# Performance work log

Hardware: AMD Instinct MI355X
Metric: run time of the kernel (lower is better)

The kernel has to match this reference:

```python
import jax, jax.numpy as jnp
import numpy as np

B, S, DIM = 2, 2048, 2048
NH, HD, HDR = 16, 128, 64
DCKV, DCQ = 512, 1536


def _lin(x, W, b):
    return x @ W.T + b


def _rotate_half(x):
    x1, x2 = jnp.split(x, 2, axis=-1)
    return jnp.concatenate([-x2, x1], axis=-1)


def _rope(x, cos, sin):
    # x: [..., s, hdr]; cos/sin: [s, hdr]
    return x * cos + _rotate_half(x) * sin


def setup_inputs() -> dict:
    key = jax.random.key(0)
    ks = jax.random.split(key, 20)
    sc = 0.02

    def w(k, shape):
        return (jax.random.normal(k, shape, jnp.float32) * sc)

    inp = {}
    inp['x'] = jax.random.normal(ks[0], (B, S, DIM), jnp.float32)
    # standard RoPE tables for the decoupled rotary dim
    inv_freq = 1.0 / (10000.0 ** (jnp.arange(0, HDR, 2, dtype=jnp.float32) / HDR))
    t = jnp.arange(S, dtype=jnp.float32)
    freqs = jnp.outer(t, inv_freq)                      # [S, HDR/2]
    emb = jnp.concatenate([freqs, freqs], axis=-1)      # [S, HDR]
    inp['freq_cos'] = jnp.cos(emb)
    inp['freq_sin'] = jnp.sin(emb)
    inp['W_dq'] = w(ks[1], (DCQ, DIM));  inp['b_dq'] = jnp.zeros((DCQ,), jnp.float32)
    inp['W_uq'] = w(ks[2], (NH * HD, DCQ)); inp['b_uq'] = jnp.zeros((NH * HD,), jnp.float32)
    inp['W_qr'] = w(ks[3], (NH * HDR, DCQ)); inp['b_qr'] = jnp.zeros((NH * HDR,), jnp.float32)
    inp['W_dkv'] = w(ks[4], (DCKV, DIM)); inp['b_dkv'] = jnp.zeros((DCKV,), jnp.float32)
    inp['W_uk'] = w(ks[5], (NH * HD, DCKV)); inp['b_uk'] = jnp.zeros((NH * HD,), jnp.float32)
    inp['W_uv'] = w(ks[6], (NH * HD, DCKV)); inp['b_uv'] = jnp.zeros((NH * HD,), jnp.float32)
    inp['W_kr'] = w(ks[7], (HDR, DIM)); inp['b_kr'] = jnp.zeros((HDR,), jnp.float32)
    inp['W_out'] = w(ks[8], (DIM, DIM)); inp['b_out'] = jnp.zeros((DIM,), jnp.float32)
    return inp


def reference(x, freq_cos, freq_sin,
              W_dq, b_dq, W_uq, b_uq, W_qr, b_qr,
              W_dkv, b_dkv, W_uk, b_uk, W_uv, b_uv,
              W_kr, b_kr, W_out, b_out):
    b, s, d = x.shape
    c_q = _lin(x, W_dq, b_dq)                                  # [b,s,dcq]
    c_kv = _lin(x, W_dkv, b_dkv)                               # [b,s,dckv]
    c_q_r = _lin(c_q, W_qr, b_qr).reshape(b, s, NH, HDR).transpose(0, 2, 1, 3)  # [b,nh,s,hdr]
    k_r = _lin(x, W_kr, b_kr)[:, None]                         # [b,1,s,hdr]
    cos = freq_cos[:s]
    sin = freq_sin[:s]
    r_q = _rope(c_q_r, cos, sin)
    r_k = _rope(k_r, cos, sin)
    r_q = r_q.transpose(0, 2, 1, 3).reshape(b, s, NH * HDR)    # [b,s,nh*hdr]
    r_k = r_k[:, 0]                                            # [b,s,hdr]
    q = jnp.concatenate([_lin(c_q, W_uq, b_uq), r_q], axis=-1)  # [b,s,nh*hd+nh*hdr]
    k_base = _lin(c_kv, W_uk, b_uk)                            # [b,s,nh*hd]
    v = _lin(c_kv, W_uv, b_uv)                                 # [b,s,nh*hd]
    r_k_exp = jnp.broadcast_to(r_k[:, :, None, :], (b, s, NH, HDR)).reshape(b, s, NH * HDR)
    k = jnp.concatenate([k_base, r_k_exp], axis=-1)
    # faithful to original: view the concat into nh chunks of (hd+hdr)
    q = q.reshape(b, s, NH, HD + HDR).transpose(0, 2, 1, 3)    # [b,nh,s,hd+hdr]
    k = k.reshape(b, s, NH, HD + HDR).transpose(0, 2, 1, 3)
    v = v.reshape(b, s, NH, HD).transpose(0, 2, 1, 3)          # [b,nh,s,hd]
    scale = 1.0 / np.float32(np.sqrt(HD + HDR))
    att = jnp.einsum('bhqd,bhkd->bhqk', q, k) * scale          # [b,nh,s,s]
    mask = jnp.tril(jnp.ones((s, s), dtype=bool))
    att = jnp.where(mask, att, jnp.float32(-jnp.inf))
    att = jax.nn.softmax(att, axis=-1)
    y = jnp.einsum('bhqk,bhkd->bhqd', att, v)                  # [b,nh,s,hd]
    y = y.transpose(0, 2, 1, 3).reshape(b, s, d)
    return _lin(y, W_out, b_out)
```

## Files before the change

kernel.cpp:

```cpp
#include <hip/hip_runtime.h>
#include <hip/hip_bf16.h>
#include <stdint.h>


typedef __bf16 bf16x8 __attribute__((ext_vector_type(8)));
typedef float  f32x4  __attribute__((ext_vector_type(4)));

__device__ __forceinline__ uint16_t f2bf(float f) {
    uint32_t u = __builtin_bit_cast(uint32_t, f);
    u = (u + 0x7FFFu + ((u >> 16) & 1u)) >> 16;
    return (uint16_t)u;
}
__device__ __forceinline__ float bf2f(uint16_t h) {
    uint32_t u = ((uint32_t)h) << 16;
    return __builtin_bit_cast(float, u);
}

typedef __attribute__((address_space(3))) uint32_t lds_u32_t;
typedef const __attribute__((address_space(1))) uint32_t glb_u32_t;

__device__ __forceinline__ void gld16(const void* g, const void* l) {
    __builtin_amdgcn_global_load_lds((glb_u32_t*)(uintptr_t)g,
                                     (lds_u32_t*)(uint32_t)(uintptr_t)l, 16, 0, 0);
}

__global__ __launch_bounds__(256)
void conv_kernel(const float* __restrict__ src, uint16_t* __restrict__ dst,
                 int n_src, int n_dst)
{
    int i = (blockIdx.x * 256 + threadIdx.x) << 2;
    if (i >= n_dst) return;
    ushort4 o;
    if (i < n_src) {
        float4 v = *(const float4*)(src + i);
        o.x = f2bf(v.x); o.y = f2bf(v.y); o.z = f2bf(v.z); o.w = f2bf(v.w);
    } else {
        o.x = 0; o.y = 0; o.z = 0; o.w = 0;
    }
    *(ushort4*)(dst + i) = o;
}

template<int MODE>
__global__ __launch_bounds__(256, 2)
void gemm_fused(const uint16_t* __restrict__ A, const uint16_t* __restrict__ W,
                const float* __restrict__ b0, const float* __restrict__ b1,
                const float* __restrict__ b2,
                const float* __restrict__ fc, const float* __restrict__ fs,
                void* __restrict__ O0, void* __restrict__ O1,
                int M, int N, int K, int lda, int s1, int s2)
{
    __shared__ __align__(16) uint16_t Alds[128 * 32];
    __shared__ __align__(16) uint16_t Blds[128 * 32];

    const int tid  = threadIdx.x;
    const int lane = tid & 63;
    const int wave = tid >> 6;
    const int wm   = wave >> 1;
    const int wn   = wave & 1;
    const int m0   = blockIdx.y << 7;
    const int n0   = blockIdx.x << 7;

    f32x4 acc[4][4];
    #pragma unroll
    for (int i = 0; i < 4; ++i)
        #pragma unroll
        for (int j = 0; j < 4; ++j)
            acc[i][j] = (f32x4){0.f, 0.f, 0.f, 0.f};

    const int r0 = (wave << 5) + (lane >> 2);
    const int ck = (lane & 3) << 3;
    const uint16_t* gA0 = A + (size_t)(m0 + r0) * lda + ck;
    const uint16_t* gA1 = gA0 + (size_t)16 * lda;
    const uint16_t* gB0 = W + (size_t)(n0 + r0) * K + ck;
    const uint16_t* gB1 = gB0 + (size_t)16 * K;
    const uint16_t* lA0 = Alds + (wave << 10);
    const uint16_t* lA1 = lA0 + 512;
    const uint16_t* lB0 = Blds + (wave << 10);
    const uint16_t* lB1 = lB0 + 512;

    const int rsel = lane & 15;
    const int g8   = (lane >> 4) << 3;

    const int nK = K >> 5;
    for (int kt = 0; kt < nK; ++kt) {
        __syncthreads();
        gld16(gA0, lA0); gld16(gA1, lA1);
        gld16(gB0, lB0); gld16(gB1, lB1);
        gA0 += 32; gA1 += 32; gB0 += 32; gB1 += 32;
        __syncthreads();

        bf16x8 af[4], bfr[4];
        #pragma unroll
        for (int i = 0; i < 4; ++i)
            af[i] = *(const bf16x8*)&Alds[(((wm << 6) + (i << 4) + rsel) << 5) + g8];
        #pragma unroll
        for (int j = 0; j < 4; ++j)
            bfr[j] = *(const bf16x8*)&Blds[(((wn << 6) + (j << 4) + rsel) << 5) + g8];

        #pragma unroll
        for (int i = 0; i < 4; ++i)
            #pragma unroll
            for (int j = 0; j < 4; ++j)
                acc[i][j] = __builtin_amdgcn_mfma_f32_16x16x32_bf16(af[i], bfr[j], acc[i][j], 0, 0, 0);
    }

    const int col = lane & 15;
    const int rg  = lane >> 4;
    #pragma unroll
    for (int i = 0; i < 4; ++i) {
        #pragma unroll
        for (int j = 0; j < 4; ++j) {
            int n = n0 + (wn << 6) + (j << 4) + col;
            if (n >= N) continue;
            float bv = (n < s1) ? b0[n] : (n < s2) ? b1[n - s1] : b2[n - s2];
            float v[4];
            #pragma unroll
            for (int r = 0; r < 4; ++r) v[r] = acc[i][j][r] + bv;
            int mbase = m0 + (wm << 6) + (i << 4) + (rg << 2);
            if (MODE == 0) {
                uint16_t* o = (uint16_t*)O0 + (size_t)mbase * N + n;
                #pragma unroll
                for (int r = 0; r < 4; ++r) o[(size_t)r * N] = f2bf(v[r]);
            } else if (MODE == 3) {
                float* o = (float*)O0 + (size_t)mbase * N + n;
                #pragma unroll
                for (int r = 0; r < 4; ++r) o[(size_t)r * N] = v[r];
            } else {
                int b = mbase >> 11, s = mbase & 2047;
                if (n < s1) {
                    int hh = n / 192, d = n - hh * 192;
                    uint16_t* o = (uint16_t*)O0 + (((size_t)(b * 16 + hh) * 2048 + s) * 192) + d;
                    #pragma unroll
                    for (int r = 0; r < 4; ++r) o[r * 192] = f2bf(v[r]);
                } else if (MODE == 4) {
                    int nn = n - s1;
                    int d  = nn & 63;
                    float bp = b1[nn ^ 32];
                    int f = 2048 + nn;
                    int head = f / 192, dq = f - head * 192;
                    uint16_t* o = (uint16_t*)O0 + (((size_t)(b * 16 + head) * 2048 + s) * 192) + dq;
                    #pragma unroll
                    for (int r = 0; r < 4; ++r) {
                        float pv  = acc[i][j ^ 2][r] + bp;
                        float rot = (d < 32) ? -pv : pv;
                        int   sl  = s + r;
                        float out = v[r] * fc[(size_t)sl * 64 + d] + rot * fs[(size_t)sl * 64 + d];
                        o[r * 192] = f2bf(out);
                    }
                } else {
                    int nn = n - s1;
                    int hh = nn >> 7, d = nn & 127;
                    ushort4 o4;
                    o4.x = f2bf(v[0]); o4.y = f2bf(v[1]); o4.z = f2bf(v[2]); o4.w = f2bf(v[3]);
                    *(ushort4*)&((uint16_t*)O1)[(((size_t)(b * 16 + hh) * 128 + d) * 2048) + s] = o4;
                }
            }
        }
    }
}

__global__ __launch_bounds__(256)
void rope_k_kernel(const uint16_t* __restrict__ raw, int ldr,
                   const float* __restrict__ fc, const float* __restrict__ fs,
                   uint16_t* __restrict__ kp)
{
    int gid = blockIdx.x * 256 + threadIdx.x;
    int m = gid >> 6, d = gid & 63;
    int b = m >> 11, s = m & 2047;
    float x  = bf2f(raw[(size_t)m * ldr + d]);
    float xo = bf2f(raw[(size_t)m * ldr + ((d < 32) ? d + 32 : d - 32)]);
    float rot = (d < 32) ? -xo : xo;
    uint16_t bv = f2bf(x * fc[s * 64 + d] + rot * fs[s * 64 + d]);
    #pragma unroll
    for (int hh = 0; hh < 16; ++hh) {
        int f = 2048 + hh * 64 + d;
        int head = f / 192, dk = f - head * 192;
        kp[(((size_t)(b * 16 + head) * 2048 + s) * 192) + dk] = bv;
    }
}

__global__ __launch_bounds__(256)
void attn_mfma5(const uint16_t* __restrict__ qp, const uint16_t* __restrict__ kp,
                const uint16_t* __restrict__ vt, uint16_t* __restrict__ yf)
{
    __shared__ uint16_t Ks[64][200];
    __shared__ uint16_t Vs[128][72];
    __shared__ uint16_t Ps[4][16][72];

    const int tid  = threadIdx.x;
    const int lane = tid & 63;
    const int w    = tid >> 6;
    const int g    = lane >> 4;
    const int li   = lane & 15;
    const int idx  = blockIdx.x;
    const int qt   = 31 - (idx >> 5);
    const int bh   = idx & 31;
    const int b    = bh >> 4;
    const int h    = bh & 15;
    const int q0   = qt << 6;

    const size_t qkb = (size_t)bh * 2048 * 192;
    const size_t vtb = (size_t)bh * 128 * 2048;
    const float scl = 0.07216878364870323f * 1.4426950408889634f;

    bf16x8 qf[6];
    #pragma unroll
    for (int kk = 0; kk < 6; ++kk)
        qf[kk] = *(const bf16x8*)(qp + qkb +
            (size_t)(q0 + (w << 4) + li) * 192 + kk * 32 + (g << 3));

    float mst[4], lst[4];
    f32x4 oacc[8];
    #pragma unroll
    for (int r = 0; r < 4; ++r) { mst[r] = -__builtin_inff(); lst[r] = 0.f; }
    #pragma unroll
    for (int ct = 0; ct < 8; ++ct) oacc[ct] = (f32x4){0.f, 0.f, 0.f, 0.f};

    for (int t = 0; t <= qt; ++t) {
        const int j0 = t << 6;
        __syncthreads();
        #pragma unroll
        for (int p = 0; p < 6; ++p) {
            int idx2 = tid + p * 256;
            int r = idx2 / 24, c8 = (idx2 - r * 24) << 3;
            *(bf16x8*)&Ks[r][c8] = *(const bf16x8*)(kp + qkb + (size_t)(j0 + r) * 192 + c8);
        }
        #pragma unroll
        for (int p = 0; p < 8; ++p) {
            int idx2 = tid + p * 256;
            int r = idx2 >> 4, c4 = (idx2 & 15) << 2;
            *(ushort4*)&Vs[r][c4] = *(const ushort4*)(vt + vtb + (size_t)r * 2048 + j0 + c4);
        }
        __syncthreads();

        f32x4 sacc[4];
        #pragma unroll
        for (int c = 0; c < 4; ++c) sacc[c] = (f32x4){0.f, 0.f, 0.f, 0.f};
        #pragma unroll
        for (int c = 0; c < 4; ++c) {
            #pragma unroll
            for (int kk = 0; kk < 6; ++kk) {
                bf16x8 kf = *(const bf16x8*)&Ks[(c << 4) + li][kk * 32 + (g << 3)];
                sacc[c] = __builtin_amdgcn_mfma_f32_16x16x32_bf16(qf[kk], kf, sacc[c], 0, 0, 0);
            }
        }

        float corr[4];
        #pragma unroll
        for (int r = 0; r < 4; ++r) {
            const int rq = q0 + (w << 4) + (g << 2) + r;
            float sv[4];
            float mx = -__builtin_inff();
            #pragma unroll
            for (int c = 0; c < 4; ++c) {
                int colk = j0 + (c << 4) + li;
                sv[c] = (colk <= rq) ? sacc[c][r] * scl : -__builtin_inff();
                mx = fmaxf(mx, sv[c]);
            }
            #pragma unroll
            for (int off = 8; off >= 1; off >>= 1) mx = fmaxf(mx, __shfl_xor(mx, off, 64));
            float mnew = fmaxf(mst[r], mx);
            corr[r] = exp2f(mst[r] - mnew);
            mst[r] = mnew;
            float psum = 0.f;
            #pragma unroll
            for (int c = 0; c < 4; ++c) {
                float p = exp2f(sv[c] - mnew);
                psum += p;
                Ps[w][(g << 2) + r][(c << 4) + li] = f2bf(p);
            }
            #pragma unroll
            for (int off = 8; off >= 1; off >>= 1) psum += __shfl_xor(psum, off, 64);
            lst[r] = lst[r] * corr[r] + psum;
        }

        #pragma unroll
        for (int ct = 0; ct < 8; ++ct)
            #pragma unroll
            for (int r = 0; r < 4; ++r) oacc[ct][r] *= corr[r];

        bf16x8 pf0 = *(const bf16x8*)&Ps[w][li][(g << 3)];
        bf16x8 pf1 = *(const bf16x8*)&Ps[w][li][32 + (g << 3)];
        #pragma unroll
        for (int ct = 0; ct < 8; ++ct) {
            bf16x8 vf0 = *(const bf16x8*)&Vs[(ct << 4) + li][(g << 3)];
            bf16x8 vf1 = *(const bf16x8*)&Vs[(ct << 4) + li][32 + (g << 3)];
            oacc[ct] = __builtin_amdgcn_mfma_f32_16x16x32_bf16(pf0, vf0, oacc[ct], 0, 0, 0);
            oacc[ct] = __builtin_amdgcn_mfma_f32_16x16x32_bf16(pf1, vf1, oacc[ct], 0, 0, 0);
        }
    }

    #pragma unroll
    for (int r = 0; r < 4; ++r) {
        float inv = 1.f / lst[r];
        int rq = q0 + (w << 4) + (g << 2) + r;
        size_t obase = ((size_t)(b * 2048 + rq) * 2048) + h * 128;
        #pragma unroll
        for (int ct = 0; ct < 8; ++ct)
            yf[obase + (ct << 4) + li] = f2bf(oacc[ct][r] * inv);
    }
}

extern "C" void kernel_launch(void* const* d_in, const int* in_sizes, int n_in,
                              void* d_out, int out_size, void* d_ws, size_t ws_size,
                              hipStream_t stream)
{
    const float* x     = (const float*)d_in[0];
    const float* fcos  = (const float*)d_in[1];
    const float* fsin  = (const float*)d_in[2];
    const float* W_dq  = (const float*)d_in[3];
    const float* b_dq  = (const float*)d_in[4];
    const float* W_uq  = (const float*)d_in[5];
    const float* b_uq  = (const float*)d_in[6];
    const float* W_qr  = (const float*)d_in[7];
    const float* b_qr  = (const float*)d_in[8];
    const float* W_dkv = (const float*)d_in[9];
    const float* b_dkv = (const float*)d_in[10];
    const float* W_uk  = (const float*)d_in[11];
    const float* b_uk  = (const float*)d_in[12];
    const float* W_uv  = (const float*)d_in[13];
    const float* b_uv  = (const float*)d_in[14];
    const float* W_kr  = (const float*)d_in[15];
    const float* b_kr  = (const float*)d_in[16];
    const float* W_out = (const float*)d_in[17];
    const float* b_out = (const float*)d_in[18];

    char* ws = (char*)d_ws;
    uint16_t* xb     = (uint16_t*)(ws + 0);
    uint16_t* Wcat2  = (uint16_t*)(ws + 0);
    uint16_t* Wcat3  = (uint16_t*)(ws + 9437184);
    uint16_t* yf     = (uint16_t*)(ws + 0);
    uint16_t* Wout_b = (uint16_t*)(ws + 16777216);
    uint16_t* qp     = (uint16_t*)(ws + 25165824);
    uint16_t* kp     = (uint16_t*)(ws + 50331648);
    uint16_t* vt     = (uint16_t*)(ws + 75497472);
    uint16_t* Wcat1  = (uint16_t*)(ws + 75497472);
    uint16_t* c_all  = (uint16_t*)(ws + 92274688);

    dim3 blk(256);
    conv_kernel<<<dim3(8192), blk, 0, stream>>>(x,     xb,                8388608, 8388608);
    conv_kernel<<<dim3(3072), blk, 0, stream>>>(W_dq,  Wcat1,             3145728, 3145728);
    conv_kernel<<<dim3(1024), blk, 0, stream>>>(W_dkv, Wcat1 + 3145728,   1048576, 1048576);
    conv_kernel<<<dim3( 256), blk, 0, stream>>>(W_kr,  Wcat1 + 4194304,    131072,  262144);
    conv_kernel<<<dim3(4096), blk, 0, stream>>>(W_out, Wout_b,            4194304, 4194304);

    gemm_fused<0><<<dim3(17, 32), blk, 0, stream>>>(
        xb, Wcat1, b_dq, b_dkv, b_kr, nullptr, nullptr, c_all, nullptr,
        4096, 2112, 2048, 2048, 1536, 2048);

    conv_kernel<<<dim3(3072), blk, 0, stream>>>(W_uq, Wcat2,             3145728, 3145728);
    conv_kernel<<<dim3(1536), blk, 0, stream>>>(W_qr, Wcat2 + 3145728,   1572864, 1572864);
    conv_kernel<<<dim3(1024), blk, 0, stream>>>(W_uk, Wcat3,             1048576, 1048576);
    conv_kernel<<<dim3(1024), blk, 0, stream>>>(W_uv, Wcat3 + 1048576,   1048576, 1048576);

    gemm_fused<4><<<dim3(24, 32), blk, 0, stream>>>(
        c_all, Wcat2, b_uq, b_qr, b_qr, fcos, fsin, qp, nullptr,
        4096, 3072, 1536, 2112, 2048, 3072);

    gemm_fused<5><<<dim3(32, 32), blk, 0, stream>>>(
        c_all + 1536, Wcat3, b_uk, b_uv, b_uv, nullptr, nullptr, kp, vt,
        4096, 4096, 512, 2112, 2048, 4096);

    rope_k_kernel<<<dim3(1024), blk, 0, stream>>>(c_all + 2048, 2112, fcos, fsin, kp);

    attn_mfma5<<<dim3(1024), blk, 0, stream>>>(qp, kp, vt, yf);

    gemm_fused<3><<<dim3(16, 32), blk, 0, stream>>>(
        yf, Wout_b, b_out, b_out, b_out, nullptr, nullptr, d_out, nullptr,
        4096, 2048, 2048, 2048, 2048, 2048);
}
```

Measured before the change: 357.4 us.

## Merge conversion launches and add lazy softmax rescaling with diagonal-only masking

Nine separate fp32-to-bf16 conversion launches are folded into two multi-segment launches to cut launch overhead. In attention, causal masking is now applied only on the diagonal tile. The online softmax also skips the row-max reduction and accumulator rescale when the new tile's max stays within 8 (log2 units) of the running max. This lazy rescaling removes shuffles and multiplies per tile but lets probabilities exceed 1 by up to 2^8 before bf16 rounding, which is a small accuracy risk.

```diff
diff --git a/kernel.cpp b/kernel.cpp
--- a/kernel.cpp
+++ b/kernel.cpp
@@ -25,19 +25,29 @@
 }
 
 __global__ __launch_bounds__(256)
-void conv_kernel(const float* __restrict__ src, uint16_t* __restrict__ dst,
-                 int n_src, int n_dst)
+void conv_multi(const float* __restrict__ s0, uint16_t* __restrict__ d0, int q0s, int q0d,
+                const float* __restrict__ s1, uint16_t* __restrict__ d1, int q1s, int q1d,
+                const float* __restrict__ s2, uint16_t* __restrict__ d2, int q2s, int q2d,
+                const float* __restrict__ s3, uint16_t* __restrict__ d3, int q3s, int q3d,
+                const float* __restrict__ s4, uint16_t* __restrict__ d4, int q4s, int q4d)
 {
-    int i = (blockIdx.x * 256 + threadIdx.x) << 2;
-    if (i >= n_dst) return;
+    int q = blockIdx.x * 256 + threadIdx.x;
+    const float* s; uint16_t* d; int qs;
+    if (q < q0d)                    { s = s0; d = d0; qs = q0s; }
+    else if ((q -= q0d) < q1d)      { s = s1; d = d1; qs = q1s; }
+    else if ((q -= q1d) < q2d)      { s = s2; d = d2; qs = q2s; }
+    else if ((q -= q2d) < q3d)      { s = s3; d = d3; qs = q3s; }
+    else if ((q -= q3d) < q4d)      { s = s4; d = d4; qs = q4s; }
+    else return;
+    int i = q << 2;
     ushort4 o;
-    if (i < n_src) {
-        float4 v = *(const float4*)(src + i);
+    if (q < qs) {
+        float4 v = *(const float4*)(s + i);
         o.x = f2bf(v.x); o.y = f2bf(v.y); o.z = f2bf(v.z); o.w = f2bf(v.w);
     } else {
         o.x = 0; o.y = 0; o.z = 0; o.w = 0;
     }
-    *(ushort4*)(dst + i) = o;
+    *(ushort4*)(d + i) = o;
 }
 
 template<int MODE>
@@ -180,7 +190,7 @@
 }
 
 __global__ __launch_bounds__(256)
-void attn_mfma5(const uint16_t* __restrict__ qp, const uint16_t* __restrict__ kp,
+void attn_mfma6(const uint16_t* __restrict__ qp, const uint16_t* __restrict__ kp,
                 const uint16_t* __restrict__ vt, uint16_t* __restrict__ yf)
 {
     __shared__ uint16_t Ks[64][200];
@@ -202,6 +212,7 @@
     const size_t qkb = (size_t)bh * 2048 * 192;
     const size_t vtb = (size_t)bh * 128 * 2048;
     const float scl = 0.07216878364870323f * 1.4426950408889634f;
+    const float NEGINF = -__builtin_inff();
 
     bf16x8 qf[6];
     #pragma unroll
@@ -212,7 +223,7 @@
     float mst[4], lst[4];
     f32x4 oacc[8];
     #pragma unroll
-    for (int r = 0; r < 4; ++r) { mst[r] = -__builtin_inff(); lst[r] = 0.f; }
+    for (int r = 0; r < 4; ++r) { mst[r] = NEGINF; lst[r] = 0.f; }
     #pragma unroll
     for (int ct = 0; ct < 8; ++ct) oacc[ct] = (f32x4){0.f, 0.f, 0.f, 0.f};
 
@@ -245,23 +256,37 @@
             }
         }
 
+        const bool diag = (t == qt);
         float corr[4];
+        bool needscale = false;
         #pragma unroll
         for (int r = 0; r < 4; ++r) {
-            const int rq = q0 + (w << 4) + (g << 2) + r;
             float sv[4];
-            float mx = -__builtin_inff();
+            float mx = NEGINF;
             #pragma unroll
             for (int c = 0; c < 4; ++c) {
-                int colk = j0 + (c << 4) + li;
-                sv[c] = (colk <= rq) ? sacc[c][r] * scl : -__builtin_inff();
-                mx = fmaxf(mx, sv[c]);
+                float s = sacc[c][r] * scl;
+                if (diag) {
+                    int colk = j0 + (c << 4) + li;
+                    int rq = q0 + (w << 4) + (g << 2) + r;
+                    s = (colk <= rq) ? s : NEGINF;
+                }
+                sv[c] = s;
+                mx = fmaxf(mx, s);
             }
-            #pragma unroll
-            for (int off = 8; off >= 1; off >>= 1) mx = fmaxf(mx, __shfl_xor(mx, off, 64));
-            float mnew = fmaxf(mst[r], mx);
-            corr[r] = exp2f(mst[r] - mnew);
+            float mold = mst[r];
+            float mnew, cr;
+            if (__all(mx <= mold + 8.f)) {
+                mnew = mold; cr = 1.f;
+            } else {
+                #pragma unroll
+                for (int off = 8; off >= 1; off >>= 1) mx = fmaxf(mx, __shfl_xor(mx, off, 64));
+                mnew = fmaxf(mold, mx);
+                cr = exp2f(mold - mnew);
+                needscale = true;
+            }
             mst[r] = mnew;
+            corr[r] = cr;
             float psum = 0.f;
             #pragma unroll
             for (int c = 0; c < 4; ++c) {
@@ -271,13 +296,15 @@
             }
             #pragma unroll
             for (int off = 8; off >= 1; off >>= 1) psum += __shfl_xor(psum, off, 64);
-            lst[r] = lst[r] * corr[r] + psum;
-        }
-
-        #pragma unroll
-        for (int ct = 0; ct < 8; ++ct)
-            #pragma unroll
-            for (int r = 0; r < 4; ++r) oacc[ct][r] *= corr[r];
+            lst[r] = lst[r] * cr + psum;
+        }
+
+        if (needscale) {
+            #pragma unroll
+            for (int ct = 0; ct < 8; ++ct)
+                #pragma unroll
+                for (int r = 0; r < 4; ++r) oacc[ct][r] *= corr[r];
+        }
 
         bf16x8 pf0 = *(const bf16x8*)&Ps[w][li][(g << 3)];
         bf16x8 pf1 = *(const bf16x8*)&Ps[w][li][32 + (g << 3)];
@@ -338,20 +365,23 @@
     uint16_t* c_all  = (uint16_t*)(ws + 92274688);
 
     dim3 blk(256);
-    conv_kernel<<<dim3(8192), blk, 0, stream>>>(x,     xb,                8388608, 8388608);
-    conv_kernel<<<dim3(3072), blk, 0, stream>>>(W_dq,  Wcat1,             3145728, 3145728);
-    conv_kernel<<<dim3(1024), blk, 0, stream>>>(W_dkv, Wcat1 + 3145728,   1048576, 1048576);
-    conv_kernel<<<dim3( 256), blk, 0, stream>>>(W_kr,  Wcat1 + 4194304,    131072,  262144);
-    conv_kernel<<<dim3(4096), blk, 0, stream>>>(W_out, Wout_b,            4194304, 4194304);
+    conv_multi<<<dim3(16640), blk, 0, stream>>>(
+        x,     xb,              2097152, 2097152,
+        W_dq,  Wcat1,            786432,  786432,
+        W_dkv, Wcat1 + 3145728,  262144,  262144,
+        W_kr,  Wcat1 + 4194304,   32768,   65536,
+        W_out, Wout_b,          1048576, 1048576);
 
     gemm_fused<0><<<dim3(17, 32), blk, 0, stream>>>(
         xb, Wcat1, b_dq, b_dkv, b_kr, nullptr, nullptr, c_all, nullptr,
         4096, 2112, 2048, 2048, 1536, 2048);
 
-    conv_kernel<<<dim3(3072), blk, 0, stream>>>(W_uq, Wcat2,             3145728, 3145728);
-    conv_kernel<<<dim3(1536), blk, 0, stream>>>(W_qr, Wcat2 + 3145728,   1572864, 1572864);
-    conv_kernel<<<dim3(1024), blk, 0, stream>>>(W_uk, Wcat3,             1048576, 1048576);
-    conv_kernel<<<dim3(1024), blk, 0, stream>>>(W_uv, Wcat3 + 1048576,   1048576, 1048576);
+    conv_multi<<<dim3(6656), blk, 0, stream>>>(
+        W_uq, Wcat2,             786432, 786432,
+        W_qr, Wcat2 + 3145728,   393216, 393216,
+        W_uk, Wcat3,             262144, 262144,
+        W_uv, Wcat3 + 1048576,   262144, 262144,
+        nullptr, nullptr, 0, 0);
 
     gemm_fused<4><<<dim3(24, 32), blk, 0, stream>>>(
         c_all, Wcat2, b_uq, b_qr, b_qr, fcos, fsin, qp, nullptr,
@@ -363,7 +393,7 @@
 
     rope_k_kernel<<<dim3(1024), blk, 0, stream>>>(c_all + 2048, 2112, fcos, fsin, kp);
 
-    attn_mfma5<<<dim3(1024), blk, 0, stream>>>(qp, kp, vt, yf);
+    attn_mfma6<<<dim3(1024), blk, 0, stream>>>(qp, kp, vt, yf);
 
     gemm_fused<3><<<dim3(16, 32), blk, 0, stream>>>(
         yf, Wout_b, b_out, b_out, b_out, nullptr, nullptr, d_out, nullptr,
```

Measured after the change: 418.0 us. +16.9%, slower.
